# Kernel tuning notes

Measured on AMD Instinct MI355X. Metric: run time of the kernel, lower is better.

The kernel has to match this reference:

```python
import jax, jax.numpy as jnp
import numpy as np

D_MODEL = 1024
N_HEADS = 16
HEAD_DIM = D_MODEL // N_HEADS
D_FF = 4096
B, S = 2, 2048
EPS = 1e-6
NEG = -1e9


def setup_inputs() -> dict:
    key = jax.random.key(0)
    ks = jax.random.split(key, 16)
    sd = 1.0 / np.sqrt(D_MODEL)
    sf = 1.0 / np.sqrt(D_FF)
    inp = {
        "x": jax.random.normal(ks[0], (B, S, D_MODEL), jnp.float32),
        # causal mask, broadcastable over batch and heads
        "mask": jnp.tril(jnp.ones((S, S), jnp.bool_))[None, None, :, :],
        # attention projections, torch Linear layout [out, in]
        "Wq": jax.random.normal(ks[1], (D_MODEL, D_MODEL), jnp.float32) * sd,
        "bq": jnp.zeros((D_MODEL,), jnp.float32),
        "Wk": jax.random.normal(ks[2], (D_MODEL, D_MODEL), jnp.float32) * sd,
        "bk": jnp.zeros((D_MODEL,), jnp.float32),
        "Wv": jax.random.normal(ks[3], (D_MODEL, D_MODEL), jnp.float32) * sd,
        "bv": jnp.zeros((D_MODEL,), jnp.float32),
        "Wo": jax.random.normal(ks[4], (D_MODEL, D_MODEL), jnp.float32) * sd,
        "bo": jnp.zeros((D_MODEL,), jnp.float32),
        # layer norms
        "ln1_g": jnp.ones((D_MODEL,), jnp.float32),
        "ln1_b": jnp.zeros((D_MODEL,), jnp.float32),
        "ln2_g": jnp.ones((D_MODEL,), jnp.float32),
        "ln2_b": jnp.zeros((D_MODEL,), jnp.float32),
        # FFN
        "W1": jax.random.normal(ks[5], (D_FF, D_MODEL), jnp.float32) * sd,
        "b1": jnp.zeros((D_FF,), jnp.float32),
        "W2": jax.random.normal(ks[6], (D_MODEL, D_FF), jnp.float32) * sf,
        "b2": jnp.zeros((D_MODEL,), jnp.float32),
    }
    return inp


def _layer_norm(x, g, b):
    mu = jnp.mean(x, axis=-1, keepdims=True)
    var = jnp.var(x, axis=-1, keepdims=True)
    return (x - mu) * jax.lax.rsqrt(var + EPS) * g + b


def _linear(x, W, b):
    return jnp.einsum('...i,oi->...o', x, W) + b


def _attention(x, mask, Wq, bq, Wk, bk, Wv, bv, Wo, bo):
    Bsz, Sq, _ = x.shape
    q = _linear(x, Wq, bq).reshape(Bsz, Sq, N_HEADS, HEAD_DIM)
    k = _linear(x, Wk, bk).reshape(Bsz, Sq, N_HEADS, HEAD_DIM)
    v = _linear(x, Wv, bv).reshape(Bsz, Sq, N_HEADS, HEAD_DIM)
    # [B,H,S,S]
    scores = jnp.einsum('bqhd,bkhd->bhqk', q, k) / np.sqrt(HEAD_DIM)
    scores = jnp.where(mask, scores, NEG)
    weights = jax.nn.softmax(scores, axis=-1)
    ctx = jnp.einsum('bhqk,bkhd->bqhd', weights, v).reshape(Bsz, Sq, D_MODEL)
    return _linear(ctx, Wo, bo)


def reference(x, mask, Wq, bq, Wk, bk, Wv, bv, Wo, bo,
              ln1_g, ln1_b, ln2_g, ln2_b, W1, b1, W2, b2):
    # pre-LN attention block (dropout = identity at inference)
    h = _layer_norm(x, ln1_g, ln1_b)
    x = x + _attention(h, mask, Wq, bq, Wk, bk, Wv, bv, Wo, bo)
    # pre-LN FFN block
    h = _layer_norm(x, ln2_g, ln2_b)
    h = jax.nn.gelu(_linear(h, W1, b1), approximate=False)
    x = x + _linear(h, W2, b2)
    return x
```

## Files before the change

### kernel.cpp

```cpp
#include <hip/hip_runtime.h>
#include <hip/hip_bf16.h>
#include <cstdint>
#include <cstddef>

typedef unsigned short u16;
typedef __bf16 bf16x8 __attribute__((ext_vector_type(8)));
typedef float f32x4 __attribute__((ext_vector_type(4)));

#define D_MODEL 1024
#define D_FF    4096
#define BATCH   2
#define SEQ     2048
#define NH      16
#define HD      64
#define ROWS    (BATCH*SEQ)
#define QKVS    3072

__device__ __forceinline__ u16 f2bf(float f) {
    union { float f; uint32_t u; } v; v.f = f;
    uint32_t u = v.u;
    u += 0x7FFF + ((u >> 16) & 1);
    return (u16)(u >> 16);
}

__device__ __forceinline__ float bf2f(u16 u) {
    union { uint32_t u; float f; } v; v.u = (uint32_t)u << 16;
    return v.f;
}

__device__ __forceinline__ uint32_t cvtpk_bf16(float lo, float hi) {
    uint32_t r;
    asm("v_cvt_pk_bf16_f32 %0, %1, %2" : "=v"(r) : "v"(lo), "v"(hi));
    return r;
}

__device__ __forceinline__ bf16x8 ldg8(const u16* p) {
    return *reinterpret_cast<const bf16x8*>(p);
}

__device__ __forceinline__ f32x4 mfma16(bf16x8 a, bf16x8 b, f32x4 c) {
    return __builtin_amdgcn_mfma_f32_16x16x32_bf16(a, b, c, 0, 0, 0);
}

__device__ __forceinline__ void gld_lds16(const void* g, void* l) {
    __builtin_amdgcn_global_load_lds(
        (const __attribute__((address_space(1))) void*)g,
        (__attribute__((address_space(3))) void*)l, 16, 0, 0);
}

__device__ __forceinline__ float gelu_f(float x) {
    float u = fmaf(0.044715f * x, x * x, x);
    float z = fminf(-2.3022036f * u, 126.0f);
    float e = __builtin_amdgcn_exp2f(z);
    return x / (1.0f + e);
}

struct alignas(8) U16x4 { u16 x, y, z, w; };

__global__ __launch_bounds__(256) void prep(
    const float* __restrict__ s0, const float* __restrict__ s1,
    const float* __restrict__ s2, const float* __restrict__ s3,
    const float* __restrict__ s4, const float* __restrict__ s5,
    u16* __restrict__ wout,
    const float* __restrict__ x, const float* __restrict__ g1,
    const float* __restrict__ be1, u16* __restrict__ hbuf,
    const float* __restrict__ bq, const float* __restrict__ bk,
    const float* __restrict__ bv, float* __restrict__ bqkv)
{
    const size_t MM1 = 1 << 20;
    const int bid = blockIdx.x;
    const int t = threadIdx.x;

    if (bid < 12288) {
        size_t i = (size_t)bid * 1024 + t * 4;
        const float* src; size_t off;
        if      (i <     MM1) { src = s0; off = i; }
        else if (i < 2 * MM1) { src = s1; off = i - MM1; }
        else if (i < 3 * MM1) { src = s2; off = i - 2 * MM1; }
        else if (i < 4 * MM1) { src = s3; off = i - 3 * MM1; }
        else if (i < 8 * MM1) { src = s4; off = i - 4 * MM1; }
        else                  { src = s5; off = i - 8 * MM1; }
        float4 f = *reinterpret_cast<const float4*>(src + off);
        U16x4 o{ f2bf(f.x), f2bf(f.y), f2bf(f.z), f2bf(f.w) };
        *reinterpret_cast<U16x4*>(wout + i) = o;
    } else if (bid < 12288 + ROWS) {
        int row = bid - 12288;
        const float* xr = x + (size_t)row * D_MODEL;
        float4 v = *reinterpret_cast<const float4*>(xr + t * 4);
        float s = v.x + v.y + v.z + v.w;
        float q = v.x*v.x + v.y*v.y + v.z*v.z + v.w*v.w;
        #pragma unroll
        for (int off = 1; off < 64; off <<= 1) {
            s += __shfl_xor(s, off);
            q += __shfl_xor(q, off);
        }
        __shared__ float red[8];
        if ((t & 63) == 0) { red[(t >> 6) * 2] = s; red[(t >> 6) * 2 + 1] = q; }
        __syncthreads();
        float sum = red[0] + red[2] + red[4] + red[6];
        float sq  = red[1] + red[3] + red[5] + red[7];
        float mu  = sum * (1.0f / D_MODEL);
        float var = sq * (1.0f / D_MODEL) - mu * mu;
        float rstd = rsqrtf(var + 1e-6f);
        float4 gg = *reinterpret_cast<const float4*>(g1 + t * 4);
        float4 bb = *reinterpret_cast<const float4*>(be1 + t * 4);
        U16x4 o{ f2bf((v.x - mu) * rstd * gg.x + bb.x),
                 f2bf((v.y - mu) * rstd * gg.y + bb.y),
                 f2bf((v.z - mu) * rstd * gg.z + bb.z),
                 f2bf((v.w - mu) * rstd * gg.w + bb.w) };
        *reinterpret_cast<U16x4*>(hbuf + (size_t)row * D_MODEL + t * 4) = o;
    } else {
        int j = bid - (12288 + ROWS);
        const float* src = (j == 0) ? bq : (j == 1) ? bk : bv;
        float4 f = *reinterpret_cast<const float4*>(src + t * 4);
        *reinterpret_cast<float4*>(bqkv + j * 1024 + t * 4) = f;
    }
}

__global__ __launch_bounds__(256) void ln_bf16(
    const float* __restrict__ x, const float* __restrict__ g,
    const float* __restrict__ b, u16* __restrict__ out)
{
    int row = blockIdx.x;
    const float* xr = x + (size_t)row * D_MODEL;
    int t = threadIdx.x;
    float4 v = *reinterpret_cast<const float4*>(xr + t * 4);
    float s = v.x + v.y + v.z + v.w;
    float q = v.x*v.x + v.y*v.y + v.z*v.z + v.w*v.w;
    #pragma unroll
    for (int off = 1; off < 64; off <<= 1) {
        s += __shfl_xor(s, off);
        q += __shfl_xor(q, off);
    }
    __shared__ float red[8];
    if ((t & 63) == 0) { red[(t >> 6) * 2] = s; red[(t >> 6) * 2 + 1] = q; }
    __syncthreads();
    float sum = red[0] + red[2] + red[4] + red[6];
    float sq  = red[1] + red[3] + red[5] + red[7];
    float mu  = sum * (1.0f / D_MODEL);
    float var = sq * (1.0f / D_MODEL) - mu * mu;
    float rstd = rsqrtf(var + 1e-6f);
    float4 gg = *reinterpret_cast<const float4*>(g + t * 4);
    float4 bb = *reinterpret_cast<const float4*>(b + t * 4);
    U16x4 o{ f2bf((v.x - mu) * rstd * gg.x + bb.x),
             f2bf((v.y - mu) * rstd * gg.y + bb.y),
             f2bf((v.z - mu) * rstd * gg.z + bb.z),
             f2bf((v.w - mu) * rstd * gg.w + bb.w) };
    *reinterpret_cast<U16x4*>(out + (size_t)row * D_MODEL + t * 4) = o;
}

#define EPI_BF16   0
#define EPI_RESF32 1
#define EPI_GELU   2
#define EPI_PART   3

template<int EPI>
__global__ __launch_bounds__(256, 4) void gemm97(
    const u16* __restrict__ A, const u16* __restrict__ B,
    const float* __restrict__ bias, const float* __restrict__ res,
    u16* __restrict__ outb, float* __restrict__ outf,
    int M, int N, int K, int KS)
{
    __shared__ u16 As[128 * 64];
    __shared__ u16 Bs[128 * 64];
    const int t = threadIdx.x;
    const int lane = t & 63, w = t >> 6;
    const int lr = lane & 15, lg = lane >> 4;
    const int wrr = (w >> 1) * 64, wcc = (w & 1) * 64;
    const int brow = blockIdx.x * 128, bcol = blockIdx.y * 128;
    const u16* Ag = A + (size_t)brow * KS;
    const u16* Bg = B + (size_t)bcol * KS;

    f32x4 acc[4][4] = {};
    const int NT = K >> 6;

    for (int kt = 0; kt < NT; ++kt) {
        #pragma unroll
        for (int c = 0; c < 4; ++c) {
            int f = c * 256 + t;
            int row = f >> 3, slot = f & 7;
            int sg = slot ^ (row & 7);
            gld_lds16(Ag + (size_t)row * KS + kt * 64 + sg * 8, As + f * 8);
            gld_lds16(Bg + (size_t)row * KS + kt * 64 + sg * 8, Bs + f * 8);
        }
        __syncthreads();

        bf16x8 af[4][2];
        #pragma unroll
        for (int mi = 0; mi < 4; ++mi) {
            int row = wrr + mi * 16 + lr;
            const u16* bp = As + row * 64;
            int key = row & 7;
            af[mi][0] = ldg8(bp + ((0 + lg) ^ key) * 8);
            af[mi][1] = ldg8(bp + ((4 + lg) ^ key) * 8);
        }
        __builtin_amdgcn_s_setprio(1);
        #pragma unroll
        for (int ni = 0; ni < 4; ++ni) {
            int row = wcc + ni * 16 + lr;
            const u16* bp = Bs + row * 64;
            int key = row & 7;
            bf16x8 b0 = ldg8(bp + ((0 + lg) ^ key) * 8);
            bf16x8 b1 = ldg8(bp + ((4 + lg) ^ key) * 8);
            #pragma unroll
            for (int mi = 0; mi < 4; ++mi) {
                acc[mi][ni] = mfma16(af[mi][0], b0, acc[mi][ni]);
                acc[mi][ni] = mfma16(af[mi][1], b1, acc[mi][ni]);
            }
        }
        __builtin_amdgcn_s_setprio(0);
        __syncthreads();
    }

    #pragma unroll
    for (int mi = 0; mi < 4; ++mi) {
        int r0 = brow + wrr + mi * 16 + lg * 4;
        #pragma unroll
        for (int ni = 0; ni < 4; ++ni) {
            int c = bcol + wcc + ni * 16 + lr;
            float bv = bias[c];
            #pragma unroll
            for (int j = 0; j < 4; ++j) {
                float v = acc[mi][ni][j] + bv;
                size_t idx = (size_t)(r0 + j) * N + c;
                if constexpr (EPI == EPI_GELU) {
                    outb[idx] = f2bf(gelu_f(v));
                } else if constexpr (EPI == EPI_RESF32) {
                    outf[idx] = v + res[idx];
                } else {
                    outb[idx] = f2bf(v);
                }
            }
        }
    }
}

template<int EPI, int RM>
__global__ __launch_bounds__(256, 2) void gemm_bt(
    const u16* __restrict__ A, const u16* __restrict__ B,
    const float* __restrict__ bias, const float* __restrict__ res,
    u16* __restrict__ outb, float* __restrict__ outf,
    int M, int N, int K, int KS)
{
    __shared__ u16 As[2][128 * 64];
    __shared__ u16 Bs[2][128 * 64];
    const int t = threadIdx.x;
    const int lane = t & 63;
    const int w = t >> 6;
    const int lr = lane & 15, lg = lane >> 4;
    const int wrr = (w >> 1) * 64, wcc = (w & 1) * 64;
    const int brow = (RM ? blockIdx.x : blockIdx.y) * 128;
    const int bcol = (RM ? blockIdx.y : blockIdx.x) * 128;
    const int kz = blockIdx.z;
    const u16* Ag = A + (size_t)brow * KS + (size_t)kz * K;
    const u16* Bg = B + (size_t)bcol * KS + (size_t)kz * K;

    f32x4 acc[4][4] = {};

    const int NT = K >> 6;

    auto stage = [&](int buf, int kt) {
        const u16* ga = Ag + kt * 64;
        const u16* gb = Bg + kt * 64;
        u16* la = As[buf];
        u16* lb = Bs[buf];
        #pragma unroll
        for (int c = 0; c < 4; ++c) {
            int f = c * 256 + t;
            int row = f >> 3, slot = f & 7;
            int sg = slot ^ (row & 7);
            gld_lds16(ga + (size_t)row * KS + sg * 8, la + f * 8);
            gld_lds16(gb + (size_t)row * KS + sg * 8, lb + f * 8);
        }
    };

    auto compute = [&](int buf) {
        const u16* la = As[buf];
        const u16* lb = Bs[buf];
        bf16x8 af[4][2];
        #pragma unroll
        for (int mi = 0; mi < 4; ++mi) {
            int row = wrr + mi * 16 + lr;
            int base = row * 64;
            af[mi][0] = *reinterpret_cast<const bf16x8*>(la + base + ((0 + lg) ^ (row & 7)) * 8);
            af[mi][1] = *reinterpret_cast<const bf16x8*>(la + base + ((4 + lg) ^ (row & 7)) * 8);
        }
        __builtin_amdgcn_s_setprio(1);
        #pragma unroll
        for (int ni = 0; ni < 4; ++ni) {
            int row = wcc + ni * 16 + lr;
            int base = row * 64;
            bf16x8 b0 = *reinterpret_cast<const bf16x8*>(lb + base + ((0 + lg) ^ (row & 7)) * 8);
            bf16x8 b1 = *reinterpret_cast<const bf16x8*>(lb + base + ((4 + lg) ^ (row & 7)) * 8);
            #pragma unroll
            for (int mi = 0; mi < 4; ++mi) {
                acc[mi][ni] = mfma16(af[mi][0], b0, acc[mi][ni]);
                acc[mi][ni] = mfma16(af[mi][1], b1, acc[mi][ni]);
            }
        }
        __builtin_amdgcn_s_setprio(0);
    };

    stage(0, 0);
    if (NT > 1) {
        stage(1, 1);
        asm volatile("s_waitcnt vmcnt(8)" ::: "memory");
    } else {
        asm volatile("s_waitcnt vmcnt(0)" ::: "memory");
    }
    __builtin_amdgcn_s_barrier();

    for (int kt = 0; kt < NT; ++kt) {
        compute(kt & 1);
        if (kt + 1 == NT) break;
        __builtin_amdgcn_s_barrier();
        if (kt + 2 < NT) {
            stage(kt & 1, kt + 2);
            asm volatile("s_waitcnt vmcnt(8)" ::: "memory");
        } else {
            asm volatile("s_waitcnt vmcnt(0)" ::: "memory");
        }
        __builtin_amdgcn_s_barrier();
    }

    #pragma unroll
    for (int mi = 0; mi < 4; ++mi) {
        int r0 = brow + wrr + mi * 16 + lg * 4;
        #pragma unroll
        for (int ni = 0; ni < 4; ++ni) {
            int c = bcol + wcc + ni * 16 + lr;
            float bv = 0.f;
            if constexpr (EPI != EPI_PART) bv = bias[c];
            #pragma unroll
            for (int j = 0; j < 4; ++j) {
                float v = acc[mi][ni][j] + bv;
                size_t idx = (size_t)(r0 + j) * N + c;
                if constexpr (EPI == EPI_GELU) {
                    outb[idx] = f2bf(gelu_f(v));
                } else if constexpr (EPI == EPI_RESF32) {
                    outf[idx] = v + res[idx];
                } else if constexpr (EPI == EPI_PART) {
                    outb[idx + (size_t)kz * M * N] = f2bf(v);
                } else {
                    outb[idx] = f2bf(v);
                }
            }
        }
    }
}

__global__ void ffn2_reduce(const u16* __restrict__ p,
                            const float* __restrict__ b2,
                            const float* __restrict__ x2,
                            float* __restrict__ out)
{
    size_t i = ((size_t)blockIdx.x * 256 + threadIdx.x) * 4;
    U16x4 a0 = *reinterpret_cast<const U16x4*>(p + i);
    U16x4 a1 = *reinterpret_cast<const U16x4*>(p + (size_t)ROWS * D_MODEL + i);
    float4 r  = *reinterpret_cast<const float4*>(x2 + i);
    float4 bb = *reinterpret_cast<const float4*>(b2 + (i & (D_MODEL - 1)));
    float4 o;
    o.x = bf2f(a0.x) + bf2f(a1.x) + r.x + bb.x;
    o.y = bf2f(a0.y) + bf2f(a1.y) + r.y + bb.y;
    o.z = bf2f(a0.z) + bf2f(a1.z) + r.z + bb.z;
    o.w = bf2f(a0.w) + bf2f(a1.w) + r.w + bb.w;
    *reinterpret_cast<float4*>(out + i) = o;
}

__global__ __launch_bounds__(256) void vtrans(
    const u16* __restrict__ QKV, u16* __restrict__ VT)
{
    __shared__ u16 tile[64][72];
    const int st = blockIdx.x * 64;
    const int bh = blockIdx.y;
    const int b = bh >> 4, h = bh & 15;
    const int t = threadIdx.x;

    #pragma unroll
    for (int c = 0; c < 2; ++c) {
        int tok = c * 32 + (t >> 3);
        int d0 = (t & 7) * 8;
        bf16x8 v = ldg8(QKV + ((size_t)(b * SEQ + st + tok)) * QKVS + 2048 + h * HD + d0);
        *reinterpret_cast<bf16x8*>(&tile[tok][d0]) = v;
    }
    __syncthreads();
    u16* dst = VT + (size_t)bh * HD * SEQ + st;
    #pragma unroll
    for (int c = 0; c < 2; ++c) {
        int d = c * 32 + (t >> 3);
        int tok0 = (t & 7) * 8;
        u16 vals[8];
        #pragma unroll
        for (int i = 0; i < 8; ++i) vals[i] = tile[tok0 + i][d];
        *reinterpret_cast<bf16x8*>(dst + (size_t)d * SEQ + tok0) =
            *reinterpret_cast<const bf16x8*>(vals);
    }
}

#define QBLK  64
#define KVBLK 64

__global__ __launch_bounds__(256, 3) void attn8(
    const u16* __restrict__ QKV, const u16* __restrict__ VT,
    u16* __restrict__ O)
{
    __shared__ u16 Ks[3][64 * 64];
    __shared__ u16 Vs[2][64 * 64];
    __shared__ u16 Pl[4][16 * 72];

    const int i  = blockIdx.x;
    const int bh = blockIdx.y;
    const int b = bh >> 4, h = bh & 15;
    const int qta = 31 - i;
    const int qtb = i;
    const int q0a = qta * QBLK, q0b = qtb * QBLK;
    const int t = threadIdx.x;
    const int lane = t & 63, w = t >> 6;
    const int lr = lane & 15, lg = lane >> 4;

    const size_t rowbase = (size_t)b * SEQ;
    const u16* Qg = QKV + rowbase * QKVS + h * HD;
    const u16* Kg = Qg + 1024;
    const u16* Vg = VT + (size_t)bh * HD * SEQ;

    const u16* qpa = Qg + (size_t)(q0a + w * 16 + lr) * QKVS;
    const u16* qpb = Qg + (size_t)(q0b + w * 16 + lr) * QKVS;
    bf16x8 qa0 = ldg8(qpa + lg * 8), qa1 = ldg8(qpa + 32 + lg * 8);
    bf16x8 qb0 = ldg8(qpb + lg * 8), qb1 = ldg8(qpb + 32 + lg * 8);

    f32x4 oa[4] = {}, ob[4] = {};
    float lsa[4] = {}, lsb[4] = {};

    const int ntiles = qta + 1;
    u16* Pw = Pl[w];
    const float SC = 0.125f * 1.44269504089f;

    auto stageK = [&](int buf, int tt) {
        const int kv0 = tt * KVBLK;
        #pragma unroll
        for (int c = 0; c < 2; ++c) {
            int f = c * 256 + t;
            int row = f >> 3, slot = f & 7;
            int sgk = slot ^ ((row >> 2) & 7);
            gld_lds16(Kg + (size_t)(kv0 + row) * QKVS + sgk * 8, Ks[buf] + f * 8);
        }
    };
    auto stageV = [&](int buf, int tt) {
        const int kv0 = tt * KVBLK;
        #pragma unroll
        for (int c = 0; c < 2; ++c) {
            int f = c * 256 + t;
            int row = f >> 3, slot = f & 7;
            int sgv = slot ^ (row & 7);
            gld_lds16(Vg + (size_t)row * SEQ + kv0 + sgv * 8, Vs[buf] + f * 8);
        }
    };

    auto qtile = [&](bf16x8 qf0, bf16x8 qf1, f32x4* o, float* ls,
                     int q0, int kv0, bool diag, const u16* kb, const u16* vb) {
        f32x4 s[4] = {};
        __builtin_amdgcn_s_setprio(1);
        #pragma unroll
        for (int ni = 0; ni < 4; ++ni) {
            int row = lr * 4 + ni;
            const u16* base = kb + row * 64;
            int key = (row >> 2) & 7;
            bf16x8 k0 = *reinterpret_cast<const bf16x8*>(base + ((0 + lg) ^ key) * 8);
            bf16x8 k1 = *reinterpret_cast<const bf16x8*>(base + ((4 + lg) ^ key) * 8);
            s[ni] = mfma16(qf0, k0, s[ni]);
            s[ni] = mfma16(qf1, k1, s[ni]);
        }
        __builtin_amdgcn_s_setprio(0);

        #pragma unroll
        for (int j = 0; j < 4; ++j) {
            int qi = q0 + w * 16 + lg * 4 + j;
            float p0 = __builtin_amdgcn_exp2f(s[0][j] * SC);
            float p1 = __builtin_amdgcn_exp2f(s[1][j] * SC);
            float p2 = __builtin_amdgcn_exp2f(s[2][j] * SC);
            float p3 = __builtin_amdgcn_exp2f(s[3][j] * SC);
            if (diag) {
                int kvb = kv0 + lr * 4;
                p0 = (kvb     <= qi) ? p0 : 0.f;
                p1 = (kvb + 1 <= qi) ? p1 : 0.f;
                p2 = (kvb + 2 <= qi) ? p2 : 0.f;
                p3 = (kvb + 3 <= qi) ? p3 : 0.f;
            }
            ls[j] += (p0 + p1) + (p2 + p3);
            uint2 pk = make_uint2(cvtpk_bf16(p0, p1), cvtpk_bf16(p2, p3));
            *reinterpret_cast<uint2*>(&Pw[(lg * 4 + j) * 72 + lr * 4]) = pk;
        }

        bf16x8 pa0 = *reinterpret_cast<const bf16x8*>(Pw + lr * 72 + lg * 8);
        bf16x8 pa1 = *reinterpret_cast<const bf16x8*>(Pw + lr * 72 + 32 + lg * 8);
        __builtin_amdgcn_s_setprio(1);
        #pragma unroll
        for (int ni = 0; ni < 4; ++ni) {
            int row = ni * 16 + lr;
            const u16* base = vb + row * 64;
            bf16x8 v0 = *reinterpret_cast<const bf16x8*>(base + ((0 + lg) ^ (row & 7)) * 8);
            bf16x8 v1 = *reinterpret_cast<const bf16x8*>(base + ((4 + lg) ^ (row & 7)) * 8);
            o[ni] = mfma16(pa0, v0, o[ni]);
            o[ni] = mfma16(pa1, v1, o[ni]);
        }
        __builtin_amdgcn_s_setprio(0);
    };

    stageV(0, 0);
    stageK(0, 0);
    stageK(1, 1);

    for (int tt = 0; tt < ntiles; ++tt) {
        __builtin_amdgcn_s_barrier();
        if (tt + 1 < ntiles) stageV((tt + 1) & 1, tt + 1);
        if (tt + 2 < ntiles) stageK((tt + 2) % 3, tt + 2);
        if (tt + 2 < ntiles)
            asm volatile("s_waitcnt vmcnt(6)" ::: "memory");
        else if (tt + 1 < ntiles)
            asm volatile("s_waitcnt vmcnt(4)" ::: "memory");
        else
            asm volatile("s_waitcnt vmcnt(0)" ::: "memory");

        const int kv0 = tt * KVBLK;
        const u16* kb = Ks[tt % 3];
        const u16* vb = Vs[tt & 1];

        qtile(qa0, qa1, oa, lsa, q0a, kv0, tt == qta, kb, vb);
        if (tt <= qtb)
            qtile(qb0, qb1, ob, lsb, q0b, kv0, tt == qtb, kb, vb);
    }

    #pragma unroll
    for (int j = 0; j < 4; ++j) {
        float va = lsa[j], vb2 = lsb[j];
        va += __shfl_xor(va, 1); vb2 += __shfl_xor(vb2, 1);
        va += __shfl_xor(va, 2); vb2 += __shfl_xor(vb2, 2);
        va += __shfl_xor(va, 4); vb2 += __shfl_xor(vb2, 4);
        va += __shfl_xor(va, 8); vb2 += __shfl_xor(vb2, 8);
        lsa[j] = va; lsb[j] = vb2;
    }

    u16* Oa = O + (rowbase + q0a + w * 16) * D_MODEL + h * HD;
    u16* Ob = O + (rowbase + q0b + w * 16) * D_MODEL + h * HD;
    #pragma unroll
    for (int j = 0; j < 4; ++j) {
        float inva = 1.0f / lsa[j];
        float invb = 1.0f / lsb[j];
        int r = (lg * 4 + j) * D_MODEL;
        #pragma unroll
        for (int ni = 0; ni < 4; ++ni) {
            Oa[r + ni * 16 + lr] = f2bf(oa[ni][j] * inva);
            Ob[r + ni * 16 + lr] = f2bf(ob[ni][j] * invb);
        }
    }
}

extern "C" void kernel_launch(void* const* d_in, const int* in_sizes, int n_in,
                              void* d_out, int out_size, void* d_ws, size_t ws_size,
                              hipStream_t stream)
{
    (void)in_sizes; (void)n_in; (void)out_size; (void)ws_size;
    const float* x   = (const float*)d_in[0];
    const float* Wq  = (const float*)d_in[2];
    const float* bq  = (const float*)d_in[3];
    const float* Wk  = (const float*)d_in[4];
    const float* bk  = (const float*)d_in[5];
    const float* Wv  = (const float*)d_in[6];
    const float* bv  = (const float*)d_in[7];
    const float* Wo  = (const float*)d_in[8];
    const float* bo  = (const float*)d_in[9];
    const float* g1  = (const float*)d_in[10];
    const float* be1 = (const float*)d_in[11];
    const float* g2  = (const float*)d_in[12];
    const float* be2 = (const float*)d_in[13];
    const float* W1  = (const float*)d_in[14];
    const float* b1  = (const float*)d_in[15];
    const float* W2  = (const float*)d_in[16];
    const float* b2  = (const float*)d_in[17];
    float* out = (float*)d_out;

    const size_t MM = 1 << 20;
    u16* Wqkv_b = (u16*)d_ws;
    u16* Wo_b = Wqkv_b + 3 * MM;
    u16* W1_b = Wo_b + MM;
    u16* W2_b = W1_b + 4 * MM;
    u16* hbuf = W2_b + 4 * MM;
    u16* QKVb = hbuf + 4 * MM;
    u16* ctx  = QKVb + 12 * MM;
    u16* ffn1 = ctx + 4 * MM;
    float* x2 = (float*)(ffn1 + 16 * MM);
    float* bqkv = (float*)(x2 + 4 * MM);
    u16* VTb = hbuf;
    u16* fpart = QKVb;

    prep<<<12288 + ROWS + 3, 256, 0, stream>>>(Wq, Wk, Wv, Wo, W1, W2, Wqkv_b,
                                               x, g1, be1, hbuf, bq, bk, bv, bqkv);

    dim3 gqkv(ROWS / 128, QKVS / 128);
    gemm97<EPI_BF16><<<gqkv, 256, 0, stream>>>(hbuf, Wqkv_b, bqkv, nullptr,
                                               QKVb, nullptr, ROWS, QKVS, 1024, 1024);

    vtrans<<<dim3(SEQ / 64, BATCH * NH), 256, 0, stream>>>(QKVb, VTb);

    dim3 ga(SEQ / QBLK / 2, BATCH * NH);
    attn8<<<ga, 256, 0, stream>>>(QKVb, VTb, ctx);

    dim3 gq(ROWS / 128, D_MODEL / 128);
    gemm_bt<EPI_RESF32, 1><<<gq, 256, 0, stream>>>(ctx, Wo_b, bo, x, nullptr, x2,
                                                   ROWS, D_MODEL, 1024, 1024);

    ln_bf16<<<ROWS, 256, 0, stream>>>(x2, g2, be2, hbuf);

    dim3 gf1(ROWS / 128, D_FF / 128);
    gemm97<EPI_GELU><<<gf1, 256, 0, stream>>>(hbuf, W1_b, b1, nullptr, ffn1, nullptr,
                                              ROWS, D_FF, 1024, 1024);

    dim3 gf2(D_MODEL / 128, ROWS / 128, 2);
    gemm_bt<EPI_PART, 0><<<gf2, 256, 0, stream>>>(ffn1, W2_b, nullptr, nullptr,
                                                  fpart, nullptr, ROWS, D_MODEL, 2048, 4096);
    ffn2_reduce<<<(ROWS * D_MODEL) / 1024, 256, 0, stream>>>(fpart, b2, x2, out);
}
```

Before: 223.5 us.

## Fuse V transpose into QKV GEMM epilogue and store residual in bf16

The QKV GEMM epilogue now writes the V columns directly in transposed [b,h,d,s] layout, so the separate vtrans kernel launch and its extra read/write of V go away. The attention-output residual stream x2 is also stored as bf16 instead of fp32, which halves its traffic in the Wo epilogue, in LN2 and in the final reduce. The cost is lower precision in the residual carried to the output, and the transposed V stores write 4 tokens per lane with a large stride, which may coalesce poorly.

```diff
diff --git a/kernel.cpp b/kernel.cpp
--- a/kernel.cpp
+++ b/kernel.cpp
@@ -117,16 +117,17 @@
     }
 }
 
-__global__ __launch_bounds__(256) void ln_bf16(
-    const float* __restrict__ x, const float* __restrict__ g,
+__global__ __launch_bounds__(256) void ln2_bf16(
+    const u16* __restrict__ x, const float* __restrict__ g,
     const float* __restrict__ b, u16* __restrict__ out)
 {
     int row = blockIdx.x;
-    const float* xr = x + (size_t)row * D_MODEL;
+    const u16* xr = x + (size_t)row * D_MODEL;
     int t = threadIdx.x;
-    float4 v = *reinterpret_cast<const float4*>(xr + t * 4);
-    float s = v.x + v.y + v.z + v.w;
-    float q = v.x*v.x + v.y*v.y + v.z*v.z + v.w*v.w;
+    U16x4 u = *reinterpret_cast<const U16x4*>(xr + t * 4);
+    float vx = bf2f(u.x), vy = bf2f(u.y), vz = bf2f(u.z), vw = bf2f(u.w);
+    float s = vx + vy + vz + vw;
+    float q = vx*vx + vy*vy + vz*vz + vw*vw;
     #pragma unroll
     for (int off = 1; off < 64; off <<= 1) {
         s += __shfl_xor(s, off);
@@ -142,10 +143,10 @@
     float rstd = rsqrtf(var + 1e-6f);
     float4 gg = *reinterpret_cast<const float4*>(g + t * 4);
     float4 bb = *reinterpret_cast<const float4*>(b + t * 4);
-    U16x4 o{ f2bf((v.x - mu) * rstd * gg.x + bb.x),
-             f2bf((v.y - mu) * rstd * gg.y + bb.y),
-             f2bf((v.z - mu) * rstd * gg.z + bb.z),
-             f2bf((v.w - mu) * rstd * gg.w + bb.w) };
+    U16x4 o{ f2bf((vx - mu) * rstd * gg.x + bb.x),
+             f2bf((vy - mu) * rstd * gg.y + bb.y),
+             f2bf((vz - mu) * rstd * gg.z + bb.z),
+             f2bf((vw - mu) * rstd * gg.w + bb.w) };
     *reinterpret_cast<U16x4*>(out + (size_t)row * D_MODEL + t * 4) = o;
 }
 
@@ -153,6 +154,8 @@
 #define EPI_RESF32 1
 #define EPI_GELU   2
 #define EPI_PART   3
+#define EPI_QKV    4
+#define EPI_RESB16 5
 
 template<int EPI>
 __global__ __launch_bounds__(256, 4) void gemm97(
@@ -219,6 +222,18 @@
         for (int ni = 0; ni < 4; ++ni) {
             int c = bcol + wcc + ni * 16 + lr;
             float bv = bias[c];
+            if constexpr (EPI == EPI_QKV) {
+                if (bcol >= 2048) {
+                    U16x4 pk{ f2bf(acc[mi][ni][0] + bv), f2bf(acc[mi][ni][1] + bv),
+                              f2bf(acc[mi][ni][2] + bv), f2bf(acc[mi][ni][3] + bv) };
+                    int d = c - 2048;
+                    int bb = r0 >> 11, s = r0 & 2047;
+                    u16* vt = (u16*)outf;
+                    *reinterpret_cast<U16x4*>(
+                        vt + ((size_t)(bb * NH + (d >> 6)) * HD + (d & 63)) * SEQ + s) = pk;
+                    continue;
+                }
+            }
             #pragma unroll
             for (int j = 0; j < 4; ++j) {
                 float v = acc[mi][ni][j] + bv;
@@ -339,6 +354,8 @@
                     outb[idx] = f2bf(gelu_f(v));
                 } else if constexpr (EPI == EPI_RESF32) {
                     outf[idx] = v + res[idx];
+                } else if constexpr (EPI == EPI_RESB16) {
+                    outb[idx] = f2bf(v + res[idx]);
                 } else if constexpr (EPI == EPI_PART) {
                     outb[idx + (size_t)kz * M * N] = f2bf(v);
                 } else {
@@ -351,50 +368,20 @@
 
 __global__ void ffn2_reduce(const u16* __restrict__ p,
                             const float* __restrict__ b2,
-                            const float* __restrict__ x2,
+                            const u16* __restrict__ x2,
                             float* __restrict__ out)
 {
     size_t i = ((size_t)blockIdx.x * 256 + threadIdx.x) * 4;
     U16x4 a0 = *reinterpret_cast<const U16x4*>(p + i);
     U16x4 a1 = *reinterpret_cast<const U16x4*>(p + (size_t)ROWS * D_MODEL + i);
-    float4 r  = *reinterpret_cast<const float4*>(x2 + i);
+    U16x4 rr = *reinterpret_cast<const U16x4*>(x2 + i);
     float4 bb = *reinterpret_cast<const float4*>(b2 + (i & (D_MODEL - 1)));
     float4 o;
-    o.x = bf2f(a0.x) + bf2f(a1.x) + r.x + bb.x;
-    o.y = bf2f(a0.y) + bf2f(a1.y) + r.y + bb.y;
-    o.z = bf2f(a0.z) + bf2f(a1.z) + r.z + bb.z;
-    o.w = bf2f(a0.w) + bf2f(a1.w) + r.w + bb.w;
+    o.x = bf2f(a0.x) + bf2f(a1.x) + bf2f(rr.x) + bb.x;
+    o.y = bf2f(a0.y) + bf2f(a1.y) + bf2f(rr.y) + bb.y;
+    o.z = bf2f(a0.z) + bf2f(a1.z) + bf2f(rr.z) + bb.z;
+    o.w = bf2f(a0.w) + bf2f(a1.w) + bf2f(rr.w) + bb.w;
     *reinterpret_cast<float4*>(out + i) = o;
-}
-
-__global__ __launch_bounds__(256) void vtrans(
-    const u16* __restrict__ QKV, u16* __restrict__ VT)
-{
-    __shared__ u16 tile[64][72];
-    const int st = blockIdx.x * 64;
-    const int bh = blockIdx.y;
-    const int b = bh >> 4, h = bh & 15;
-    const int t = threadIdx.x;
-
-    #pragma unroll
-    for (int c = 0; c < 2; ++c) {
-        int tok = c * 32 + (t >> 3);
-        int d0 = (t & 7) * 8;
-        bf16x8 v = ldg8(QKV + ((size_t)(b * SEQ + st + tok)) * QKVS + 2048 + h * HD + d0);
-        *reinterpret_cast<bf16x8*>(&tile[tok][d0]) = v;
-    }
-    __syncthreads();
-    u16* dst = VT + (size_t)bh * HD * SEQ + st;
-    #pragma unroll
-    for (int c = 0; c < 2; ++c) {
-        int d = c * 32 + (t >> 3);
-        int tok0 = (t & 7) * 8;
-        u16 vals[8];
-        #pragma unroll
-        for (int i = 0; i < 8; ++i) vals[i] = tile[tok0 + i][d];
-        *reinterpret_cast<bf16x8*>(dst + (size_t)d * SEQ + tok0) =
-            *reinterpret_cast<const bf16x8*>(vals);
-    }
 }
 
 #define QBLK  64
@@ -588,28 +575,26 @@
     u16* QKVb = hbuf + 4 * MM;
     u16* ctx  = QKVb + 12 * MM;
     u16* ffn1 = ctx + 4 * MM;
-    float* x2 = (float*)(ffn1 + 16 * MM);
+    u16* x2   = ffn1 + 16 * MM;
     float* bqkv = (float*)(x2 + 4 * MM);
-    u16* VTb = hbuf;
+    u16* VTb  = (u16*)(bqkv + 4096);
     u16* fpart = QKVb;
 
     prep<<<12288 + ROWS + 3, 256, 0, stream>>>(Wq, Wk, Wv, Wo, W1, W2, Wqkv_b,
                                                x, g1, be1, hbuf, bq, bk, bv, bqkv);
 
     dim3 gqkv(ROWS / 128, QKVS / 128);
-    gemm97<EPI_BF16><<<gqkv, 256, 0, stream>>>(hbuf, Wqkv_b, bqkv, nullptr,
-                                               QKVb, nullptr, ROWS, QKVS, 1024, 1024);
-
-    vtrans<<<dim3(SEQ / 64, BATCH * NH), 256, 0, stream>>>(QKVb, VTb);
+    gemm97<EPI_QKV><<<gqkv, 256, 0, stream>>>(hbuf, Wqkv_b, bqkv, nullptr,
+                                              QKVb, (float*)VTb, ROWS, QKVS, 1024, 1024);
 
     dim3 ga(SEQ / QBLK / 2, BATCH * NH);
     attn8<<<ga, 256, 0, stream>>>(QKVb, VTb, ctx);
 
     dim3 gq(ROWS / 128, D_MODEL / 128);
-    gemm_bt<EPI_RESF32, 1><<<gq, 256, 0, stream>>>(ctx, Wo_b, bo, x, nullptr, x2,
+    gemm_bt<EPI_RESB16, 1><<<gq, 256, 0, stream>>>(ctx, Wo_b, bo, x, x2, nullptr,
                                                    ROWS, D_MODEL, 1024, 1024);
 
-    ln_bf16<<<ROWS, 256, 0, stream>>>(x2, g2, be2, hbuf);
+    ln2_bf16<<<ROWS, 256, 0, stream>>>(x2, g2, be2, hbuf);
 
     dim3 gf1(ROWS / 128, D_FF / 128);
     gemm97<EPI_GELU><<<gf1, 256, 0, stream>>>(hbuf, W1_b, b1, nullptr, ffn1, nullptr,
```

Result: faster. 215.6 us (median of 2 runs) (-3.5%).
